# Performance work log

Measured on AMD Instinct MI355X. Metric: run time of the kernel, lower is better.

## Reference

```python
import jax, jax.numpy as jnp
import numpy as np

E, B, S, C, N, D, DFF, H, K_FREQ = 4, 16, 256, 17, 16, 32, 64, 4, 4
DH = D // H
MA_KERNELS = (4, 8, 12)


def setup_inputs() -> dict:
    key = jax.random.key(0)
    ks = jax.random.split(key, 16)
    sc = 1.0 / np.sqrt(D).astype(np.float32)
    inp = {
        "x": jax.random.normal(ks[0], (B, S, C, 1), jnp.float32),
        "original_x": jax.random.uniform(ks[1], (B, S, 2), jnp.float32),
        "start_W": jax.random.normal(ks[2], (D,), jnp.float32),
        "start_b": jnp.zeros((D,), jnp.float32),
        "Wq": jax.random.normal(ks[3], (E, D, D), jnp.float32) * sc,
        "Wk": jax.random.normal(ks[4], (E, D, D), jnp.float32) * sc,
        "Wv": jax.random.normal(ks[5], (E, D, D), jnp.float32) * sc,
        "Wo": jax.random.normal(ks[6], (E, D, D), jnp.float32) * sc,
        "ln1_g": jnp.ones((E, D), jnp.float32),
        "ln1_b": jnp.zeros((E, D), jnp.float32),
        "ln2_g": jnp.ones((E, D), jnp.float32),
        "ln2_b": jnp.zeros((E, D), jnp.float32),
        "W1": jax.random.normal(ks[7], (E, D, DFF), jnp.float32) * sc,
        "b1": jnp.zeros((E, DFF), jnp.float32),
        "W2": jax.random.normal(ks[8], (E, DFF, D), jnp.float32) * (1.0 / np.sqrt(DFF).astype(np.float32)),
        "b2": jnp.zeros((E, D), jnp.float32),
    }
    return inp


def _moving_avg(x, k):
    # x: [B,S,Ch], replicate-pad then uniform window of size k (stride 1)
    front = jnp.repeat(x[:, :1], (k - 1) // 2, axis=1)
    end = jnp.repeat(x[:, -1:], k // 2, axis=1)
    xp = jnp.concatenate([front, x, end], axis=1)  # [B, S+k-1, Ch]
    c = jnp.cumsum(xp, axis=1)
    c = jnp.concatenate([jnp.zeros_like(c[:, :1]), c], axis=1)
    return (c[:, k:] - c[:, :-k]) / jnp.asarray(k, x.dtype)


def _fourier_season(x, k):
    # ETSformer-style FourierLayer: keep top-k amplitude frequencies (excluding DC)
    s = x.shape[1]
    xf = jnp.fft.rfft(x, axis=1)            # [B,F,Ch] complex
    amp = jnp.abs(xf)
    amp = amp.at[:, 0, :].set(-jnp.inf)     # exclude DC
    topv = jax.lax.top_k(jnp.moveaxis(amp, 1, -1), k)[0]  # [B,Ch,k]
    thresh = topv[..., -1]                  # [B,Ch]
    mask = amp >= thresh[:, None, :]
    xf_m = jnp.where(mask, xf, 0)
    return jnp.fft.irfft(xf_m, n=s, axis=1).astype(x.dtype)


def _ln(z, g, b):
    m = jnp.mean(z, -1, keepdims=True)
    v = jnp.var(z, -1, keepdims=True)
    return (z - m) * jax.lax.rsqrt(v + 1e-5) * g + b


def _expert_fwd(args):
    h, wq, wk, wv, wo, g1, bg1, g2, bg2, w1, b1e, w2, b2e = args
    # h: [B,S,N,D]; pre-LN MHA over the sequence axis per (batch, node)
    z = _ln(h, g1, bg1)
    q = jnp.einsum('bsnd,de->bsne', z, wq).reshape(B, S, N, H, DH)
    k_ = jnp.einsum('bsnd,de->bsne', z, wk).reshape(B, S, N, H, DH)
    v_ = jnp.einsum('bsnd,de->bsne', z, wv).reshape(B, S, N, H, DH)
    att = jnp.einsum('bqnhd,bknhd->bnhqk', q, k_) * (1.0 / np.sqrt(DH).astype(np.float32))
    att = jax.nn.softmax(att, axis=-1)
    o = jnp.einsum('bnhqk,bknhd->bqnhd', att, v_).reshape(B, S, N, D)
    h = h + jnp.einsum('bsnd,de->bsne', o, wo)
    z2 = _ln(h, g2, bg2)
    f = jax.nn.relu(jnp.einsum('bsnd,df->bsnf', z2, w1) + b1e)
    h = h + jnp.einsum('bsnf,fd->bsnd', f, w2) + b2e
    return h


def reference(x, original_x, start_W, start_b, Wq, Wk, Wv, Wo,
              ln1_g, ln1_b, ln2_g, ln2_b, W1, b1, W2, b2):
    xc = x[:, :, :, 0]                                  # [B,S,C]
    trend = sum(_moving_avg(xc, k) for k in MA_KERNELS) / float(len(MA_KERNELS))
    season = _fourier_season(xc, K_FREQ)
    new_x = xc + season + trend                         # [B,S,C]

    scores = original_x[:, :, -1]                       # [B,S]
    bins = jnp.linspace(scores.min(), scores.max(), E + 1)
    assign = jnp.clip(jnp.searchsorted(bins, scores, side='right') - 1, 0, E - 1)  # [B,S] int

    xns = new_x[:, :, :-1]                              # [B,S,N] drop score channel
    onehot = (assign[None] == jnp.arange(E)[:, None, None])          # [E,B,S] bool
    expert_in = xns[None] * onehot[..., None].astype(xns.dtype)      # [E,B,S,N] dense zero-padded dispatch
    hidden = expert_in[..., None] * start_W + start_b                # [E,B,S,N,D] start_linear

    outs = jax.lax.map(_expert_fwd, (hidden, Wq, Wk, Wv, Wo,
                                     ln1_g, ln1_b, ln2_g, ln2_b, W1, b1, W2, b2))  # [E,B,S,N,D]
    combined = jnp.einsum('ebs,ebsnd->bsnd', onehot.astype(outs.dtype), outs)      # one-hot combine
    return combined
```

## Files before the change

kernel.cpp:

```cpp
#include <hip/hip_runtime.h>
#include <hip/hip_fp16.h>
#include <math.h>

#define BB 16
#define SS 256
#define CC 17
#define NCH 16
#define DD 32
#define DFFN 64
#define HH 4
#define DH 8
#define EE 4

#define WS_K0 16
#define WS_V0 144
#define WS_XNS 512
#define WS_SPI (WS_XNS + BB*SS*NCH)
#define WS_WT  (WS_SPI + BB*SS + 64)
#define WS_WL  (WS_WT + 6144)

#define PRE 0.51006977f

typedef __fp16 hv2 __attribute__((ext_vector_type(2)));

__device__ __forceinline__ unsigned pkh2(float a, float b) {
  hv2 r = __builtin_amdgcn_cvt_pkrtz(a, b);
  unsigned u; __builtin_memcpy(&u, &r, 4);
  return u;
}
__device__ __forceinline__ float fd2(unsigned a, unsigned b, float c) {
  hv2 av, bv;
  __builtin_memcpy(&av, &a, 4);
  __builtin_memcpy(&bv, &b, 4);
  return __builtin_amdgcn_fdot2(av, bv, c, false);
}
__device__ __forceinline__ __half2 u2h2(unsigned u) {
  __half2 h; __builtin_memcpy(&h, &u, 4); return h;
}

__launch_bounds__(1024)
__global__ void decomp_prep_kernel(const float* __restrict__ x,
                                   const float* __restrict__ ox,
                                   const float* __restrict__ sb,
                                   const float* __restrict__ g1,
                                   const float* __restrict__ bb1,
                                   const float* __restrict__ Wq,
                                   const float* __restrict__ Wk,
                                   const float* __restrict__ Wv,
                                   const float* __restrict__ Wo,
                                   const float* __restrict__ W1,
                                   const float* __restrict__ W2,
                                   float* __restrict__ ws) {
  const int t = threadIdx.x;
  if (blockIdx.x < 256) {
    const int b = blockIdx.x / NCH;
    const int c = blockIdx.x % NCH;
    __shared__ float xs[SS];
    __shared__ float prr[1024], pii[1024];
    __shared__ float amp[129];
    __shared__ float2 YY[129];
    __shared__ float sth;
    if (t < SS) xs[t] = x[(b*SS + t)*CC + c];
    __syncthreads();
    const float TH0 = 0.024543692606170259f;
    {
      const int f = (t & 127) + 1;
      const int chunk = t >> 7;
      const int s0 = chunk * 32;
      const int ph0 = (f * s0) & 255;
      float si, cr; sincosf(TH0*(float)ph0, &si, &cr);
      float s1, c1; sincosf(TH0*(float)f, &s1, &c1);
      float xr = 0.f, xi = 0.f;
      #pragma unroll 4
      for (int k = 0; k < 32; ++k) {
        float xvv = xs[s0 + k];
        xr += xvv * cr;
        xi -= xvv * si;
        float nc = cr*c1 - si*s1;
        si = si*c1 + cr*s1;
        cr = nc;
      }
      prr[t] = xr; pii[t] = xi;
    }
    __syncthreads();
    if (t < 128) {
      float xr = 0.f, xi = 0.f;
      #pragma unroll
      for (int k2 = 0; k2 < 8; ++k2) { xr += prr[t + 128*k2]; xi += pii[t + 128*k2]; }
      prr[t] = xr; pii[t] = xi;
      amp[t+1] = sqrtf(xr*xr + xi*xi);
    }
    __syncthreads();
    if (t < 64) {
      float a0 = amp[t+1], a1 = amp[t+65];
      int i0 = t+1, i1 = t+65;
      float th = -1e30f;
      for (int r = 0; r < 4; ++r) {
        float mv = (a0 > a1) ? a0 : a1;
        int   mi = (a0 > a1) ? i0 : i1;
        for (int off = 32; off > 0; off >>= 1) {
          float ov = __shfl_xor(mv, off);
          int   oi = __shfl_xor(mi, off);
          if (ov > mv || (ov == mv && oi < mi)) { mv = ov; mi = oi; }
        }
        th = mv;
        if (mi == i0) a0 = -1e30f;
        if (mi == i1) a1 = -1e30f;
      }
      if (t == 0) sth = th;
    }
    __syncthreads();
    if (t < 128) {
      const int f = t + 1;
      float wgt = (amp[f] >= sth) ? ((f == 128) ? 1.0f : 2.0f) * (1.0f/256.0f) : 0.0f;
      YY[f] = make_float2(wgt * prr[t], wgt * pii[t]);
    }
    __syncthreads();
    {
      const int s = t & 255;
      const int fc = t >> 8;
      const int f0 = 1 + fc*32;
      const int ph0 = (s * f0) & 255;
      float si, cr; sincosf(TH0*(float)ph0, &si, &cr);
      float s1, c1; sincosf(TH0*(float)s, &s1, &c1);
      float acc = 0.f;
      #pragma unroll 4
      for (int k = 0; k < 32; ++k) {
        float2 y = YY[f0 + k];
        acc += y.x*cr - y.y*si;
        float nc = cr*c1 - si*s1;
        si = si*c1 + cr*s1;
        cr = nc;
      }
      prr[t] = acc;
    }
    __syncthreads();
    if (t < 256) {
      float season = prr[t] + prr[t+256] + prr[t+512] + prr[t+768];
      float s4 = 0.f, s8 = 0.f, s12 = 0.f;
      #pragma unroll
      for (int j = 0; j < 4; ++j)  { int p = t + j - 1; p = p < 0 ? 0 : (p > SS-1 ? SS-1 : p); s4  += xs[p]; }
      #pragma unroll
      for (int j = 0; j < 8; ++j)  { int p = t + j - 3; p = p < 0 ? 0 : (p > SS-1 ? SS-1 : p); s8  += xs[p]; }
      #pragma unroll
      for (int j = 0; j < 12; ++j) { int p = t + j - 5; p = p < 0 ? 0 : (p > SS-1 ? SS-1 : p); s12 += xs[p]; }
      float trend = (s4 * 0.25f + s8 * 0.125f + s12 * (1.0f/12.0f)) * (1.0f/3.0f);
      ws[WS_XNS + (b*SS + t)*NCH + c] = xs[t] + season + trend;
    }
  } else if (blockIdx.x < 272) {
    const int b = blockIdx.x - 256;
    __shared__ float red[32];
    __shared__ int asg[SS];
    __shared__ int cnt[EE];
    __shared__ float z0[EE*DD];
    float mn = 3e38f, mx = -3e38f;
    #pragma unroll
    for (int k = 0; k < 4; ++k) {
      float v = ox[(t + k*1024)*2 + 1];
      mn = fminf(mn, v); mx = fmaxf(mx, v);
    }
    for (int off = 32; off > 0; off >>= 1) {
      mn = fminf(mn, __shfl_xor(mn, off));
      mx = fmaxf(mx, __shfl_xor(mx, off));
    }
    if ((t & 63) == 0) { red[(t>>6)*2] = mn; red[(t>>6)*2+1] = mx; }
    __syncthreads();
    mn = red[0]; mx = red[1];
    #pragma unroll
    for (int w = 1; w < 16; ++w) { mn = fminf(mn, red[w*2]); mx = fmaxf(mx, red[w*2+1]); }
    const float step = (mx - mn) * 0.25f;
    const float e1 = mn + step, e2 = mn + 2.f*step, e3 = mn + 3.f*step;
    if (t < 256) {
      float sc = ox[(b*SS + t)*2 + 1];
      asg[t] = (sc >= e1) + (sc >= e2) + (sc >= e3);
    }
    __syncthreads();
    if (t < EE) {
      int c = 0;
      for (int s2 = 0; s2 < SS; ++s2) c += (asg[s2] == t);
      cnt[t] = c;
    }
    __syncthreads();
    int* SPw  = (int*)ws + WS_SPI;
    int* OFFw = SPw + BB*SS;
    if (t < EE) {
      int off = 0;
      for (int i = 0; i < t; ++i) off += cnt[i];
      OFFw[b*EE + t] = off;
      int kp = off;
      for (int s2 = 0; s2 < SS; ++s2) if (asg[s2] == t) SPw[b*SS + (kp++)] = s2;
    }
    if (t < 128) {
      int ee = t >> 5, d = t & 31;
      float m = 0.f;
      for (int i = 0; i < DD; ++i) m += sb[i];
      m *= (1.0f/DD);
      float var = 0.f;
      for (int i = 0; i < DD; ++i) { float df = sb[i]-m; var += df*df; }
      var *= (1.0f/DD);
      float rs = rsqrtf(var + 1e-5f);
      z0[ee*DD + d] = (sb[d]-m)*rs*g1[ee*DD+d] + bb1[ee*DD+d];
    }
    __syncthreads();
    if (b == 0 && t < 128) {
      int ee = t >> 5, d = t & 31;
      float k0 = 0.f, v0 = 0.f;
      for (int i = 0; i < DD; ++i) {
        float zz = z0[ee*DD + i];
        k0 += zz * Wk[ee*DD*DD + i*DD + d];
        v0 += zz * Wv[ee*DD*DD + i*DD + d];
      }
      ws[WS_K0 + ee*DD + d] = k0;
      ws[WS_V0 + ee*DD + d] = v0;
    }
  } else {
    unsigned* img = (unsigned*)ws + WS_WT;
    const int base_u = (blockIdx.x - 272)*4096;
    #pragma unroll
    for (int i = 0; i < 4; ++i) {
      int u = base_u + i*1024 + t;
      unsigned val;
      if (u < 6144) {
        int mat = u >> 11, r = u & 2047;
        int row = r >> 4, ip = r & 15;
        int e = row >> 5, q = row & 31;
        int d = (q & 3)*8 + (q >> 2);
        const float* Wm = (mat == 0) ? Wq : (mat == 1) ? Wk : Wv;
        const float* src = Wm + e*1024 + d;
        val = pkh2(src[ip*64], src[ip*64 + 32]);
      } else {
        int v = u - 6144;
        if (v < 2048) {
          int row = v >> 4, ip = v & 15;
          int e = row >> 5, q = row & 31;
          int d = (q & 3)*8 + (q >> 2);
          const float* src = Wo + e*1024 + d;
          val = pkh2(src[ip*64], src[ip*64 + 32]);
        } else if (v < 6144) {
          int r = v - 2048;
          int row = r >> 4, ip = r & 15;
          int e = row >> 6, q = row & 63;
          int j = (q & 3)*16 + (q >> 2);
          const float* src = W1 + e*2048 + j;
          val = pkh2(src[ip*128], src[ip*128 + 64]);
        } else {
          int r = v - 6144;
          int a = r >> 11, rr = r & 2047;
          int row = rr >> 4, ip = rr & 15;
          int e = row >> 5, q = row & 31;
          int d = (q & 3)*8 + (q >> 2);
          int jp = a*16 + ip;
          const float* src = W2 + e*2048 + d;
          val = pkh2(src[2*jp*32], src[(2*jp+1)*32]);
        }
      }
      img[u] = val;
    }
  }
}

__launch_bounds__(1024, 4)
__global__ void fused_kernel(const float* __restrict__ ws,
    const float* __restrict__ g1, const float* __restrict__ bb1,
    const float* __restrict__ sW, const float* __restrict__ sb,
    const float* __restrict__ g2, const float* __restrict__ bb2,
    const float* __restrict__ b1, const float* __restrict__ b2,
    float* __restrict__ out) {
  const int blk = blockIdx.x;
  const int n = blk & 15;
  const int b = blk >> 4;
  const int t = threadIdx.x;
  const int p = t >> 2;
  const int hh = t & 3;
  __shared__ unsigned lds[24576];
  float* fl = (float*)lds;
  unsigned* wT = lds + 8192;
  unsigned* wl = lds + 14336;

  {
    const unsigned* img = (const unsigned*)ws + WS_WT;
    const int wv = t >> 6;
    const int ln = t & 63;
    #pragma unroll
    for (int i = 0; i < 4; ++i) {
      const int ch = wv*4 + i;
      __builtin_amdgcn_global_load_lds(
          (const __attribute__((address_space(1))) unsigned*)(img + ch*256 + ln*4),
          (__attribute__((address_space(3))) unsigned*)(wT + ch*256 + ln*4),
          16, 0, 0);
    }
  }

  const int* SP  = (const int*)ws + WS_SPI;
  const int* OFF = SP + BB*SS;
  const int o1 = OFF[b*4+1], o2v = OFF[b*4+2], o3 = OFF[b*4+3];
  const int e = (p >= o1) + (p >= o2v) + (p >= o3);
  const int beg = (e==0) ? 0  : ((e==1) ? o1 : ((e==2) ? o2v : o3));
  const int end = (e==0) ? o1 : ((e==1) ? o2v : ((e==2) ? o3 : SS));
  const int s = SP[b*SS + p];
  const float xv = ws[WS_XNS + (b*SS + s)*NCH + n];

  float h[DD];
  #pragma unroll
  for (int d = 0; d < DD; ++d) h[d] = xv * sW[d] + sb[d];
  float m = 0.f;
  #pragma unroll
  for (int d = 0; d < DD; ++d) m += h[d];
  m *= (1.0f/DD);
  float var = 0.f;
  #pragma unroll
  for (int d = 0; d < DD; ++d) { float df = h[d]-m; var += df*df; }
  var *= (1.0f/DD);
  float rs = rsqrtf(var + 1e-5f);
  unsigned zp[16];
  #pragma unroll
  for (int ip = 0; ip < 16; ++ip) {
    float za = (h[2*ip]  -m)*rs*g1[e*DD+2*ip]   + bb1[e*DD+2*ip];
    float zb = (h[2*ip+1]-m)*rs*g1[e*DD+2*ip+1] + bb1[e*DD+2*ip+1];
    zp[ip] = pkh2(za, zb);
  }
  __syncthreads();

  float q[DH], kk[DH], vv[DH];
  #pragma unroll
  for (int dd = 0; dd < DH; ++dd) {
    const int row16 = (e*32 + dd*4 + hh)*16;
    const uint4* rq = (const uint4*)&wT[row16];
    const uint4* rk = (const uint4*)&wT[2048 + row16];
    const uint4* rv = (const uint4*)&wT[4096 + row16];
    float aq = 0.f, ak = 0.f, av = 0.f;
    #pragma unroll
    for (int g4 = 0; g4 < 4; ++g4) {
      uint4 wq4 = rq[g4], wk4 = rk[g4], wv4 = rv[g4];
      aq = fd2(zp[4*g4+0], wq4.x, aq); aq = fd2(zp[4*g4+1], wq4.y, aq);
      aq = fd2(zp[4*g4+2], wq4.z, aq); aq = fd2(zp[4*g4+3], wq4.w, aq);
      ak = fd2(zp[4*g4+0], wk4.x, ak); ak = fd2(zp[4*g4+1], wk4.y, ak);
      ak = fd2(zp[4*g4+2], wk4.z, ak); ak = fd2(zp[4*g4+3], wk4.w, ak);
      av = fd2(zp[4*g4+0], wv4.x, av); av = fd2(zp[4*g4+1], wv4.y, av);
      av = fd2(zp[4*g4+2], wv4.z, av); av = fd2(zp[4*g4+3], wv4.w, av);
    }
    q[dd] = aq * PRE; kk[dd] = ak; vv[dd] = av;
  }
  *(uint4*)&lds[p*32 + hh*8]     = make_uint4(pkh2(kk[0],kk[1]), pkh2(kk[2],kk[3]),
                                              pkh2(kk[4],kk[5]), pkh2(kk[6],kk[7]));
  *(uint4*)&lds[p*32 + hh*8 + 4] = make_uint4(pkh2(vv[0],vv[1]), pkh2(vv[2],vv[3]),
                                              pkh2(vv[4],vv[5]), pkh2(vv[6],vv[7]));
  unsigned qp2[4];
  #pragma unroll
  for (int i = 0; i < 4; ++i) qp2[i] = pkh2(q[2*i], q[2*i+1]);
  float s0 = 0.f;
  #pragma unroll
  for (int d = 0; d < DH; ++d) s0 += q[d] * ws[WS_K0 + e*DD + hh*DH + d];
  __syncthreads();

  float wsum = 0.f;
  __half2 o2[4];
  #pragma unroll
  for (int i = 0; i < 4; ++i) o2[i] = u2h2(0u);
  int jk = beg;
  for (; jk + 1 < end; jk += 2) {
    uint4 ku0 = *(const uint4*)&lds[jk*32 + hh*8];
    uint4 vu0 = *(const uint4*)&lds[jk*32 + hh*8 + 4];
    uint4 ku1 = *(const uint4*)&lds[(jk+1)*32 + hh*8];
    uint4 vu1 = *(const uint4*)&lds[(jk+1)*32 + hh*8 + 4];
    float a0 = 0.f, a1 = 0.f;
    a0 = fd2(qp2[0], ku0.x, a0); a0 = fd2(qp2[1], ku0.y, a0);
    a0 = fd2(qp2[2], ku0.z, a0); a0 = fd2(qp2[3], ku0.w, a0);
    a1 = fd2(qp2[0], ku1.x, a1); a1 = fd2(qp2[1], ku1.y, a1);
    a1 = fd2(qp2[2], ku1.z, a1); a1 = fd2(qp2[3], ku1.w, a1);
    float w0f = __builtin_amdgcn_exp2f(a0);
    float w1f = __builtin_amdgcn_exp2f(a1);
    wsum += w0f + w1f;
    __half2 w20 = u2h2(pkh2(w0f, w0f));
    __half2 w21 = u2h2(pkh2(w1f, w1f));
    o2[0] = __hfma2(w20, u2h2(vu0.x), o2[0]);
    o2[1] = __hfma2(w20, u2h2(vu0.y), o2[1]);
    o2[2] = __hfma2(w20, u2h2(vu0.z), o2[2]);
    o2[3] = __hfma2(w20, u2h2(vu0.w), o2[3]);
    o2[0] = __hfma2(w21, u2h2(vu1.x), o2[0]);
    o2[1] = __hfma2(w21, u2h2(vu1.y), o2[1]);
    o2[2] = __hfma2(w21, u2h2(vu1.z), o2[2]);
    o2[3] = __hfma2(w21, u2h2(vu1.w), o2[3]);
  }
  if (jk < end) {
    uint4 ku = *(const uint4*)&lds[jk*32 + hh*8];
    uint4 vu = *(const uint4*)&lds[jk*32 + hh*8 + 4];
    float a = 0.f;
    a = fd2(qp2[0], ku.x, a); a = fd2(qp2[1], ku.y, a);
    a = fd2(qp2[2], ku.z, a); a = fd2(qp2[3], ku.w, a);
    float wf = __builtin_amdgcn_exp2f(a);
    wsum += wf;
    __half2 w2 = u2h2(pkh2(wf, wf));
    o2[0] = __hfma2(w2, u2h2(vu.x), o2[0]);
    o2[1] = __hfma2(w2, u2h2(vu.y), o2[1]);
    o2[2] = __hfma2(w2, u2h2(vu.z), o2[2]);
    o2[3] = __hfma2(w2, u2h2(vu.w), o2[3]);
  }
  float o[DH];
  #pragma unroll
  for (int i = 0; i < 4; ++i) {
    o[2*i]   = __low2float(o2[i]);
    o[2*i+1] = __high2float(o2[i]);
  }
  const int nmis = SS - (end - beg);
  float w0 = (float)nmis * __builtin_amdgcn_exp2f(s0);
  wsum += w0;
  #pragma unroll
  for (int d = 0; d < DH; ++d) o[d] += w0 * ws[WS_V0 + e*DD + hh*DH + d];
  float inv = 1.0f / wsum;
  #pragma unroll
  for (int d = 0; d < DH; ++d) o[d] *= inv;
  __syncthreads();

  #pragma unroll
  for (int d = 0; d < DH; ++d) fl[p*33 + hh*DH + d] = o[d];
  __syncthreads();
  unsigned ovp[16];
  #pragma unroll
  for (int ip = 0; ip < 16; ++ip) ovp[ip] = pkh2(fl[p*33 + 2*ip], fl[p*33 + 2*ip+1]);

  float acc[DH];
  #pragma unroll
  for (int dd = 0; dd < DH; ++dd) {
    int d = hh*DH + dd;
    const uint4* row = (const uint4*)&wl[(e*32 + dd*4 + hh)*16];
    float a = xv * sW[d] + sb[d];
    #pragma unroll
    for (int g4 = 0; g4 < 4; ++g4) {
      uint4 w4 = row[g4];
      a = fd2(ovp[4*g4+0], w4.x, a); a = fd2(ovp[4*g4+1], w4.y, a);
      a = fd2(ovp[4*g4+2], w4.z, a); a = fd2(ovp[4*g4+3], w4.w, a);
    }
    acc[dd] = a;
  }
  __syncthreads();
  #pragma unroll
  for (int dd = 0; dd < DH; ++dd) fl[p*33 + hh*DH + dd] = acc[dd];
  __syncthreads();

  float h2r[DD];
  #pragma unroll
  for (int i = 0; i < DD; ++i) h2r[i] = fl[p*33 + i];
  m = 0.f;
  #pragma unroll
  for (int d = 0; d < DD; ++d) m += h2r[d];
  m *= (1.0f/DD);
  var = 0.f;
  #pragma unroll
  for (int d = 0; d < DD; ++d) { float df = h2r[d]-m; var += df*df; }
  var *= (1.0f/DD);
  rs = rsqrtf(var + 1e-5f);
  unsigned zp2[16];
  #pragma unroll
  for (int ip = 0; ip < 16; ++ip) {
    float za = (h2r[2*ip]  -m)*rs*g2[e*DD+2*ip]   + bb2[e*DD+2*ip];
    float zb = (h2r[2*ip+1]-m)*rs*g2[e*DD+2*ip+1] + bb2[e*DD+2*ip+1];
    zp2[ip] = pkh2(za, zb);
  }
  float hres[DH];
  #pragma unroll
  for (int dd = 0; dd < DH; ++dd) hres[dd] = h2r[hh*DH + dd];
  __syncthreads();

  float f[16];
  #pragma unroll
  for (int jj = 0; jj < 16; ++jj) {
    const uint4* row = (const uint4*)&wl[2048 + (e*64 + jj*4 + hh)*16];
    float a = b1[e*DFFN + hh*16 + jj];
    #pragma unroll
    for (int g4 = 0; g4 < 4; ++g4) {
      uint4 w4 = row[g4];
      a = fd2(zp2[4*g4+0], w4.x, a); a = fd2(zp2[4*g4+1], w4.y, a);
      a = fd2(zp2[4*g4+2], w4.z, a); a = fd2(zp2[4*g4+3], w4.w, a);
    }
    f[jj] = fmaxf(a, 0.0f);
  }
  {
    uint4 fa = make_uint4(pkh2(f[0],f[1]), pkh2(f[2],f[3]), pkh2(f[4],f[5]), pkh2(f[6],f[7]));
    uint4 fb = make_uint4(pkh2(f[8],f[9]), pkh2(f[10],f[11]), pkh2(f[12],f[13]), pkh2(f[14],f[15]));
    *(uint4*)&lds[p*36 + hh*8]     = fa;
    *(uint4*)&lds[p*36 + hh*8 + 4] = fb;
  }
  __syncthreads();

  uint4 fpr[8];
  #pragma unroll
  for (int g4 = 0; g4 < 8; ++g4) fpr[g4] = *(const uint4*)&lds[p*36 + 4*g4];
  float acc2[DH];
  #pragma unroll
  for (int dd = 0; dd < DH; ++dd) {
    int d = hh*DH + dd;
    const int row16 = (e*32 + dd*4 + hh)*16;
    float a = hres[dd] + b2[e*DD + d];
    #pragma unroll
    for (int g4 = 0; g4 < 8; ++g4) {
      const int plane = (g4 >> 2);
      uint4 w4 = *(const uint4*)&wl[6144 + plane*2048 + row16 + 4*(g4 & 3)];
      uint4 fq = fpr[g4];
      a = fd2(fq.x, w4.x, a); a = fd2(fq.y, w4.y, a);
      a = fd2(fq.z, w4.z, a); a = fd2(fq.w, w4.w, a);
    }
    acc2[dd] = a;
  }
  float* op = out + ((size_t)((b*SS + s)*NCH + n))*DD + hh*DH;
  *(float4*)(op)     = make_float4(acc2[0], acc2[1], acc2[2], acc2[3]);
  *(float4*)(op + 4) = make_float4(acc2[4], acc2[5], acc2[6], acc2[7]);
}

extern "C" void kernel_launch(void* const* d_in, const int* in_sizes, int n_in,
                              void* d_out, int out_size, void* d_ws, size_t ws_size,
                              hipStream_t stream) {
  (void)in_sizes; (void)n_in; (void)out_size; (void)ws_size;
  const float* x   = (const float*)d_in[0];
  const float* ox  = (const float*)d_in[1];
  const float* sW  = (const float*)d_in[2];
  const float* sb  = (const float*)d_in[3];
  const float* Wq  = (const float*)d_in[4];
  const float* Wk  = (const float*)d_in[5];
  const float* Wv  = (const float*)d_in[6];
  const float* Wo  = (const float*)d_in[7];
  const float* g1  = (const float*)d_in[8];
  const float* b1n = (const float*)d_in[9];
  const float* g2  = (const float*)d_in[10];
  const float* b2n = (const float*)d_in[11];
  const float* W1  = (const float*)d_in[12];
  const float* bf1 = (const float*)d_in[13];
  const float* W2  = (const float*)d_in[14];
  const float* bf2 = (const float*)d_in[15];
  float* out = (float*)d_out;
  float* ws  = (float*)d_ws;

  decomp_prep_kernel<<<276, 1024, 0, stream>>>(x, ox, sb, g1, b1n,
                                               Wq, Wk, Wv, Wo, W1, W2, ws);
  fused_kernel<<<BB*NCH, 1024, 0, stream>>>(ws, g1, b1n, sW, sb, g2, b2n,
                                            bf1, bf2, out);
}
```

Before: 139.0 us.

## Replace LDS exchanges and barriers with DPP quad broadcasts and reductions

The four threads that share a token position now exchange their packed fp16 slices of the attention output, the LayerNorm input and the FFN hidden vector through DPP quad-permute moves instead of writing to LDS and reading back between __syncthreads barriers. The LayerNorm mean and variance become quad-level DPP butterfly reductions over each thread's 8 elements, so the full 32-wide row no longer has to be gathered. This removes several block-wide barriers and LDS round trips per token. In exchange it adds more cross-lane move instructions, and it relies on the four threads of a position sitting in adjacent lanes of the same quad.

```diff
diff --git a/kernel.cpp b/kernel.cpp
--- a/kernel.cpp
+++ b/kernel.cpp
@@ -36,6 +36,14 @@
 }
 __device__ __forceinline__ __half2 u2h2(unsigned u) {
   __half2 h; __builtin_memcpy(&h, &u, 4); return h;
+}
+template<int PAT>
+__device__ __forceinline__ unsigned qdpp(unsigned v) {
+  return (unsigned)__builtin_amdgcn_mov_dpp((int)v, PAT, 0xF, 0xF, true);
+}
+template<int PAT>
+__device__ __forceinline__ float qdppf(float v) {
+  return __uint_as_float(qdpp<PAT>(__float_as_uint(v)));
 }
 
 __launch_bounds__(1024)
@@ -273,7 +281,6 @@
   const int p = t >> 2;
   const int hh = t & 3;
   __shared__ unsigned lds[24576];
-  float* fl = (float*)lds;
   unsigned* wT = lds + 8192;
   unsigned* wl = lds + 14336;
 
@@ -410,14 +417,18 @@
   float inv = 1.0f / wsum;
   #pragma unroll
   for (int d = 0; d < DH; ++d) o[d] *= inv;
-  __syncthreads();
-
-  #pragma unroll
-  for (int d = 0; d < DH; ++d) fl[p*33 + hh*DH + d] = o[d];
-  __syncthreads();
+
+  unsigned oq[4];
+  #pragma unroll
+  for (int j = 0; j < 4; ++j) oq[j] = pkh2(o[2*j], o[2*j+1]);
   unsigned ovp[16];
   #pragma unroll
-  for (int ip = 0; ip < 16; ++ip) ovp[ip] = pkh2(fl[p*33 + 2*ip], fl[p*33 + 2*ip+1]);
+  for (int j = 0; j < 4; ++j) {
+    ovp[j]    = qdpp<0x00>(oq[j]);
+    ovp[4+j]  = qdpp<0x55>(oq[j]);
+    ovp[8+j]  = qdpp<0xAA>(oq[j]);
+    ovp[12+j] = qdpp<0xFF>(oq[j]);
+  }
 
   float acc[DH];
   #pragma unroll
@@ -433,34 +444,35 @@
     }
     acc[dd] = a;
   }
-  __syncthreads();
-  #pragma unroll
-  for (int dd = 0; dd < DH; ++dd) fl[p*33 + hh*DH + dd] = acc[dd];
-  __syncthreads();
-
-  float h2r[DD];
-  #pragma unroll
-  for (int i = 0; i < DD; ++i) h2r[i] = fl[p*33 + i];
-  m = 0.f;
-  #pragma unroll
-  for (int d = 0; d < DD; ++d) m += h2r[d];
-  m *= (1.0f/DD);
-  var = 0.f;
-  #pragma unroll
-  for (int d = 0; d < DD; ++d) { float df = h2r[d]-m; var += df*df; }
-  var *= (1.0f/DD);
-  rs = rsqrtf(var + 1e-5f);
+
+  float ssum = 0.f;
+  #pragma unroll
+  for (int dd = 0; dd < DH; ++dd) ssum += acc[dd];
+  ssum += qdppf<0xB1>(ssum);
+  ssum += qdppf<0x4E>(ssum);
+  float m2 = ssum * (1.0f/DD);
+  float vs = 0.f;
+  #pragma unroll
+  for (int dd = 0; dd < DH; ++dd) { float df = acc[dd]-m2; vs += df*df; }
+  vs += qdppf<0xB1>(vs);
+  vs += qdppf<0x4E>(vs);
+  float rs2 = rsqrtf(vs * (1.0f/DD) + 1e-5f);
+  unsigned zq[4];
+  #pragma unroll
+  for (int j = 0; j < 4; ++j) {
+    int d = hh*DH + 2*j;
+    float za = (acc[2*j]  -m2)*rs2*g2[e*DD+d]   + bb2[e*DD+d];
+    float zb = (acc[2*j+1]-m2)*rs2*g2[e*DD+d+1] + bb2[e*DD+d+1];
+    zq[j] = pkh2(za, zb);
+  }
   unsigned zp2[16];
   #pragma unroll
-  for (int ip = 0; ip < 16; ++ip) {
-    float za = (h2r[2*ip]  -m)*rs*g2[e*DD+2*ip]   + bb2[e*DD+2*ip];
-    float zb = (h2r[2*ip+1]-m)*rs*g2[e*DD+2*ip+1] + bb2[e*DD+2*ip+1];
-    zp2[ip] = pkh2(za, zb);
-  }
-  float hres[DH];
-  #pragma unroll
-  for (int dd = 0; dd < DH; ++dd) hres[dd] = h2r[hh*DH + dd];
-  __syncthreads();
+  for (int j = 0; j < 4; ++j) {
+    zp2[j]    = qdpp<0x00>(zq[j]);
+    zp2[4+j]  = qdpp<0x55>(zq[j]);
+    zp2[8+j]  = qdpp<0xAA>(zq[j]);
+    zp2[12+j] = qdpp<0xFF>(zq[j]);
+  }
 
   float f[16];
   #pragma unroll
@@ -475,30 +487,30 @@
     }
     f[jj] = fmaxf(a, 0.0f);
   }
-  {
-    uint4 fa = make_uint4(pkh2(f[0],f[1]), pkh2(f[2],f[3]), pkh2(f[4],f[5]), pkh2(f[6],f[7]));
-    uint4 fb = make_uint4(pkh2(f[8],f[9]), pkh2(f[10],f[11]), pkh2(f[12],f[13]), pkh2(f[14],f[15]));
-    *(uint4*)&lds[p*36 + hh*8]     = fa;
-    *(uint4*)&lds[p*36 + hh*8 + 4] = fb;
-  }
-  __syncthreads();
-
-  uint4 fpr[8];
-  #pragma unroll
-  for (int g4 = 0; g4 < 8; ++g4) fpr[g4] = *(const uint4*)&lds[p*36 + 4*g4];
+  unsigned fq[8];
+  #pragma unroll
+  for (int j = 0; j < 8; ++j) fq[j] = pkh2(f[2*j], f[2*j+1]);
+  unsigned fu[32];
+  #pragma unroll
+  for (int j = 0; j < 8; ++j) {
+    fu[j]    = qdpp<0x00>(fq[j]);
+    fu[8+j]  = qdpp<0x55>(fq[j]);
+    fu[16+j] = qdpp<0xAA>(fq[j]);
+    fu[24+j] = qdpp<0xFF>(fq[j]);
+  }
+
   float acc2[DH];
   #pragma unroll
   for (int dd = 0; dd < DH; ++dd) {
     int d = hh*DH + dd;
     const int row16 = (e*32 + dd*4 + hh)*16;
-    float a = hres[dd] + b2[e*DD + d];
+    float a = acc[dd] + b2[e*DD + d];
     #pragma unroll
     for (int g4 = 0; g4 < 8; ++g4) {
       const int plane = (g4 >> 2);
       uint4 w4 = *(const uint4*)&wl[6144 + plane*2048 + row16 + 4*(g4 & 3)];
-      uint4 fq = fpr[g4];
-      a = fd2(fq.x, w4.x, a); a = fd2(fq.y, w4.y, a);
-      a = fd2(fq.z, w4.z, a); a = fd2(fq.w, w4.w, a);
+      a = fd2(fu[4*g4+0], w4.x, a); a = fd2(fu[4*g4+1], w4.y, a);
+      a = fd2(fu[4*g4+2], w4.z, a); a = fd2(fu[4*g4+3], w4.w, a);
     }
     acc2[dd] = a;
   }
```

Result: faster. 134.4 us (median of 2 runs) (-3.3%).
